# Kernel optimization log

Measured on AMD Instinct MI355X. Metric: run time of the kernel, lower is better.

The kernel has to match this reference:

```python
import jax, jax.numpy as jnp
import numpy as np
from jax import lax

DIM = 512
ATT_DIM = 512
N_HEADS = 8
HEAD_DIM = ATT_DIM // N_HEADS
SEQ = 4096


def q_rsqrt(x):
    # quake-style fast inverse sqrt with one Newton iteration (matches torch module)
    y = np.asarray((x,), dtype=np.float32)
    x2 = y * 0.5
    i = y.view(np.int32)
    i = np.right_shift(i, 1)
    i = 1597463007 - i
    y = i.view(np.float32)
    y = y * (1.5 - x2 * y * y)
    return float(y[0])

SCALING = q_rsqrt(HEAD_DIM)  # fast-approx 1/sqrt(head_dim)

# Schraudolph fast-exp constants (pulp-trainlib fastexp_gist)
GIST_A = 12102203.17133801  # 2^23 / ln(2)
GIST_B = 1064986823.0       # bias with correction term
GIST_C = 8388608.0          # underflow cutoff -> 0
GIST_D = 2139095040.0       # overflow clamp (float32 inf bits)


def fastexp_gist(x):
    t = GIST_A * x + GIST_B
    t = jnp.where(t < GIST_C, 0.0, jnp.where(t > GIST_D, GIST_D, t))
    return lax.bitcast_convert_type(t.astype(jnp.int32), jnp.float32)


def softmax_fastexp(s):
    m = jnp.max(s, axis=-1, keepdims=True)
    e = fastexp_gist(s - m)
    return e / jnp.sum(e, axis=-1, keepdims=True)


def setup_inputs() -> dict:
    key = jax.random.key(0)
    ks = jax.random.split(key, 8)
    std = 0.02
    return {
        "x": jax.random.normal(ks[0], (SEQ, DIM), dtype=jnp.float32),
        "Wq": jax.random.normal(ks[1], (ATT_DIM, DIM), dtype=jnp.float32) * std,
        "bq": jnp.zeros((ATT_DIM,), dtype=jnp.float32),
        "Wk": jax.random.normal(ks[2], (ATT_DIM, DIM), dtype=jnp.float32) * std,
        "bk": jnp.zeros((ATT_DIM,), dtype=jnp.float32),
        "Wv": jax.random.normal(ks[3], (ATT_DIM, DIM), dtype=jnp.float32) * std,
        "bv": jnp.zeros((ATT_DIM,), dtype=jnp.float32),
        "Wout": jax.random.normal(ks[4], (DIM, ATT_DIM), dtype=jnp.float32) * std,
        "tgt_len": SEQ,
    }


def reference(x, Wq, bq, Wk, bk, Wv, bv, Wout, tgt_len):
    # projections (torch Linear: y = x @ W.T + b)
    q = (x @ Wq.T + bq).reshape(tgt_len, N_HEADS, HEAD_DIM).transpose(1, 0, 2)  # [H,L,d]
    k = (x @ Wk.T + bk).reshape(tgt_len, N_HEADS, HEAD_DIM).transpose(1, 0, 2)
    v = (x @ Wv.T + bv).reshape(tgt_len, N_HEADS, HEAD_DIM).transpose(1, 0, 2)
    scores = jnp.einsum('hld,hmd->hlm', q, k) * SCALING  # [H,L,L]
    probs = softmax_fastexp(scores)
    out = jnp.einsum('hlm,hmd->hld', probs, v)           # [H,L,d]
    out = out.transpose(1, 0, 2).reshape(tgt_len, ATT_DIM)
    return out @ Wout.T  # proj_out has no bias
```

## Files before the change

kernel.cpp:

```cpp
#include <hip/hip_runtime.h>
#include <hip/hip_bf16.h>
#include <string.h>

#define SEQ 4096
#define DIM 512
#define NH  8
#define HD  64
#define SEQP (SEQ + 128)
#define NT  (SEQ/64)
#define KSPLIT 4
#define KCHUNK (SEQ/KSPLIT)
#define KTILES (KCHUNK/64)

typedef __attribute__((ext_vector_type(4))) float  f32x4;
typedef __attribute__((ext_vector_type(8))) short  bf16x8;
typedef __attribute__((ext_vector_type(4))) short  s16x4;
typedef __attribute__((ext_vector_type(2))) unsigned int u32x2;

__device__ __forceinline__ unsigned short f2bfh(float f){
    union { __hip_bfloat16 h; unsigned short u; } cv;
    cv.h = __float2bfloat16(f);
    return cv.u;
}

__device__ __forceinline__ bf16x8 cvt8(f32x4 lo, f32x4 hi){
    bf16x8 r;
    r[0]=(short)f2bfh(lo[0]); r[1]=(short)f2bfh(lo[1]);
    r[2]=(short)f2bfh(lo[2]); r[3]=(short)f2bfh(lo[3]);
    r[4]=(short)f2bfh(hi[0]); r[5]=(short)f2bfh(hi[1]);
    r[6]=(short)f2bfh(hi[2]); r[7]=(short)f2bfh(hi[3]);
    return r;
}

__device__ __forceinline__ bf16x8 load8f(const float* p){
    f32x4 lo = *(const f32x4*)p;
    f32x4 hi = *(const f32x4*)(p+4);
    return cvt8(lo, hi);
}

#define FENCE_LDS() asm volatile("s_waitcnt lgkmcnt(0)" ::: "memory")

__global__ __launch_bounds__(256) void cvt5_kernel(
    const float* __restrict__ x,  const float* __restrict__ wq,
    const float* __restrict__ wk, const float* __restrict__ wv,
    const float* __restrict__ wo,
    unsigned short* __restrict__ xb,  unsigned short* __restrict__ wqb,
    unsigned short* __restrict__ wkb, unsigned short* __restrict__ wvb,
    unsigned short* __restrict__ wob)
{
    int b = blockIdx.x;
    const float* src; unsigned short* dst; int base;
    if (b < 1024){ src = x; dst = xb; base = b; }
    else {
        int t  = (b - 1024) >> 7;
        base   = (b - 1024) & 127;
        src = (t==0) ? wq  : (t==1) ? wk  : (t==2) ? wv  : wo;
        dst = (t==0) ? wqb : (t==1) ? wkb : (t==2) ? wvb : wob;
    }
    size_t i = ((size_t)base*256 + threadIdx.x)*8;
    f32x4 lo = *(const f32x4*)(src + i);
    f32x4 hi = *(const f32x4*)(src + i + 4);
    *(bf16x8*)(dst + i) = cvt8(lo, hi);
}

__global__ __launch_bounds__(256, 4) void proj_qkv_b_kernel(
    const unsigned short* __restrict__ xb,
    const unsigned short* __restrict__ Wqb, const float* __restrict__ bq,
    const unsigned short* __restrict__ Wkb, const float* __restrict__ bk,
    const unsigned short* __restrict__ Wvb, const float* __restrict__ bv,
    unsigned short* __restrict__ Qb, unsigned short* __restrict__ Kh,
    unsigned short* __restrict__ Vtp)
{
    __shared__ __align__(16) unsigned short xs[128*64];
    __shared__ __align__(16) unsigned short wsh[64*64];

    const int z = blockIdx.z;
    const unsigned short* W = (z==0) ? Wqb : ((z==1) ? Wkb : Wvb);
    const float* bb = (z==0) ? bq : ((z==1) ? bk : bv);
    const int tid = threadIdx.x;
    const int wv  = tid >> 6;
    const int l   = tid & 63;
    const int g   = l >> 4;
    const int l15 = l & 15;
    const int l7  = l15 & 7;
    const int r0b = blockIdx.x * 128;
    const int c0  = blockIdx.y * 64;
    const int hy  = blockIdx.y;

    const int sc  = tid & 7;
    const int sr  = tid >> 3;
    const int scs = (sc ^ (sr & 7)) * 8;

    f32x4 acc[2][4];
    #pragma unroll
    for(int s=0;s<2;s++)
        #pragma unroll
        for(int d=0;d<4;d++) acc[s][d] = (f32x4){0.f,0.f,0.f,0.f};

    bf16x8 xf[4], wf[2];
    #pragma unroll
    for(int j=0;j<4;j++)
        xf[j] = *(const bf16x8*)(xb + (size_t)(r0b + sr + 32*j)*DIM + sc*8);
    #pragma unroll
    for(int j=0;j<2;j++)
        wf[j] = *(const bf16x8*)(W + (size_t)(c0 + sr + 32*j)*DIM + sc*8);

    for(int t=0;t<8;t++){
        #pragma unroll
        for(int j=0;j<4;j++)
            *(bf16x8*)&xs[(sr + 32*j)*64 + scs] = xf[j];
        #pragma unroll
        for(int j=0;j<2;j++)
            *(bf16x8*)&wsh[(sr + 32*j)*64 + scs] = wf[j];
        __syncthreads();
        if(t+1 < 8){
            const int kt = (t+1)*64;
            #pragma unroll
            for(int j=0;j<4;j++)
                xf[j] = *(const bf16x8*)(xb + (size_t)(r0b + sr + 32*j)*DIM + kt + sc*8);
            #pragma unroll
            for(int j=0;j<2;j++)
                wf[j] = *(const bf16x8*)(W + (size_t)(c0 + sr + 32*j)*DIM + kt + sc*8);
        }
        #pragma unroll
        for(int kh=0;kh<2;kh++){
            bf16x8 a[2];
            #pragma unroll
            for(int s=0;s<2;s++){
                const int row = wv*32 + s*16 + l15;
                a[s] = *(const bf16x8*)&xs[row*64 + (((kh*4+g) ^ l7)*8)];
            }
            #pragma unroll
            for(int d=0;d<4;d++){
                const int row = d*16 + l15;
                bf16x8 b = *(const bf16x8*)&wsh[row*64 + (((kh*4+g) ^ l7)*8)];
                #pragma unroll
                for(int s=0;s<2;s++)
                    acc[s][d] = __builtin_amdgcn_mfma_f32_16x16x32_bf16(a[s], b, acc[s][d], 0,0,0);
            }
        }
        __syncthreads();
    }

    const int r0 = r0b + wv*32;
    #pragma unroll
    for(int d=0;d<4;d++){
        float bias = bb[c0 + d*16 + l15];
        #pragma unroll
        for(int s=0;s<2;s++){
            if(z == 2){
                s16x4 pk;
                #pragma unroll
                for(int r=0;r<4;r++) pk[r] = (short)f2bfh(acc[s][d][r] + bias);
                *(s16x4*)(Vtp + ((size_t)hy*HD + d*16+l15)*SEQP + r0 + s*16 + g*4) = pk;
            } else if(z == 1){
                #pragma unroll
                for(int r=0;r<4;r++)
                    Kh[((size_t)hy*SEQ + r0+s*16+g*4+r)*HD + d*16 + l15] =
                        f2bfh(acc[s][d][r] + bias);
            } else {
                #pragma unroll
                for(int r=0;r<4;r++)
                    Qb[(size_t)(r0+s*16+g*4+r)*DIM + c0 + d*16 + l15] =
                        f2bfh(acc[s][d][r] + bias);
            }
        }
    }
}

__global__ __launch_bounds__(256) void proj_qkv_kernel(
    const float* __restrict__ x,
    const float* __restrict__ Wq, const float* __restrict__ bq,
    const float* __restrict__ Wk, const float* __restrict__ bk,
    const float* __restrict__ Wv, const float* __restrict__ bv,
    unsigned short* __restrict__ Qb, unsigned short* __restrict__ Kh,
    unsigned short* __restrict__ Vtp)
{
    const int z = blockIdx.z;
    const float* W  = (z==0) ? Wq : ((z==1) ? Wk : Wv);
    const float* bb = (z==0) ? bq : ((z==1) ? bk : bv);
    const int wv  = threadIdx.x >> 6;
    const int l   = threadIdx.x & 63;
    const int g   = l >> 4;
    const int l15 = l & 15;
    const int r0  = blockIdx.x * 128 + wv * 32;
    const int c0  = blockIdx.y * 64;
    const int hy  = blockIdx.y;

    f32x4 acc[2][4];
    #pragma unroll
    for(int s=0;s<2;s++)
        #pragma unroll
        for(int d=0;d<4;d++) acc[s][d] = (f32x4){0.f,0.f,0.f,0.f};

    for(int kt=0; kt<DIM; kt+=32){
        bf16x8 a[2];
        #pragma unroll
        for(int s=0;s<2;s++)
            a[s] = load8f(x + (size_t)(r0+s*16+l15)*DIM + kt + g*8);
        #pragma unroll
        for(int d=0;d<4;d++){
            bf16x8 b = load8f(W + (size_t)(c0+d*16+l15)*DIM + kt + g*8);
            #pragma unroll
            for(int s=0;s<2;s++)
                acc[s][d] = __builtin_amdgcn_mfma_f32_16x16x32_bf16(a[s], b, acc[s][d], 0,0,0);
        }
    }

    #pragma unroll
    for(int d=0;d<4;d++){
        float bias = bb[c0 + d*16 + l15];
        #pragma unroll
        for(int s=0;s<2;s++){
            if(z == 2){
                s16x4 pk;
                #pragma unroll
                for(int r=0;r<4;r++) pk[r] = (short)f2bfh(acc[s][d][r] + bias);
                *(s16x4*)(Vtp + ((size_t)hy*HD + d*16+l15)*SEQP + r0 + s*16 + g*4) = pk;
            } else if(z == 1){
                #pragma unroll
                for(int r=0;r<4;r++)
                    Kh[((size_t)hy*SEQ + r0+s*16+g*4+r)*HD + d*16 + l15] =
                        f2bfh(acc[s][d][r] + bias);
            } else {
                #pragma unroll
                for(int r=0;r<4;r++)
                    Qb[(size_t)(r0+s*16+g*4+r)*DIM + c0 + d*16 + l15] =
                        f2bfh(acc[s][d][r] + bias);
            }
        }
    }
}

__global__ __launch_bounds__(512, 4) void attn_max_kernel(
    const unsigned short* __restrict__ Qb,
    const unsigned short* __restrict__ Kh,
    float* __restrict__ Pm)
{
    __shared__ __align__(16) unsigned short kb[2][64*64];

    const int tid = threadIdx.x;
    const int wv  = tid >> 6;
    const int l   = tid & 63;
    const int g   = l >> 4;
    const int l15 = l & 15;
    const int l7  = l15 & 7;
    const int h   = blockIdx.x & 7;
    const int kz  = (blockIdx.x >> 3) & 3;
    const int Rw  = (blockIdx.x >> 5) * 256 + wv * 32;
    const int kbase = kz * KCHUNK;

    const unsigned short* Khh = Kh + (size_t)h*SEQ*HD;
    const int sr  = tid >> 3, sc = tid & 7;
    const int scs = (sc ^ (sr & 7)) * 8;
    const int lA  = sr*64 + scs;

    bf16x8 aq[2][2];
    #pragma unroll
    for(int s=0;s<2;s++)
        #pragma unroll
        for(int kh=0;kh<2;kh++)
            aq[s][kh] = *(const bf16x8*)(Qb + (size_t)(Rw+s*16+l15)*DIM + h*HD + kh*32 + g*8);

    float mx[2];
    mx[0] = mx[1] = -3.0e38f;

    bf16x8 krA = *(const bf16x8*)(Khh + (size_t)(kbase+sr)*HD + sc*8);
    *(bf16x8*)&kb[0][lA] = krA;
    __syncthreads();

    for(int t=0;t<KTILES;t++){
        const int cur = t & 1;
        if(t+1 < KTILES)
            krA = *(const bf16x8*)(Khh + (size_t)(kbase+(t+1)*64+sr)*HD + sc*8);
        #pragma unroll
        for(int ks=0;ks<4;ks++){
            const int krow = ks*16 + l15;
            bf16x8 b0 = *(const bf16x8*)&kb[cur][krow*64 + ((g     ^ l7)*8)];
            bf16x8 b1 = *(const bf16x8*)&kb[cur][krow*64 + (((4+g) ^ l7)*8)];
            __builtin_amdgcn_s_setprio(1);
            #pragma unroll
            for(int s=0;s<2;s++){
                f32x4 acc = (f32x4){0.f,0.f,0.f,0.f};
                acc = __builtin_amdgcn_mfma_f32_16x16x32_bf16(b0, aq[s][0], acc, 0,0,0);
                acc = __builtin_amdgcn_mfma_f32_16x16x32_bf16(b1, aq[s][1], acc, 0,0,0);
                #pragma unroll
                for(int r=0;r<4;r++) mx[s] = fmaxf(mx[s], acc[r]);
            }
            __builtin_amdgcn_s_setprio(0);
        }
        if(t+1 < KTILES)
            *(bf16x8*)&kb[cur^1][lA] = krA;
        __syncthreads();
    }
    #pragma unroll
    for(int s=0;s<2;s++){
        mx[s] = fmaxf(mx[s], __shfl_xor(mx[s], 16, 64));
        mx[s] = fmaxf(mx[s], __shfl_xor(mx[s], 32, 64));
    }

    if(l < 16){
        Pm[(size_t)(h*KSPLIT + kz)*SEQ + Rw + l15]      = mx[0];
        Pm[(size_t)(h*KSPLIT + kz)*SEQ + Rw + 16 + l15] = mx[1];
    }
}

#define PSTRIDE 68

__global__ __launch_bounds__(512, 4) void attn_pv_kernel(
    const unsigned short* __restrict__ Qb,
    const unsigned short* __restrict__ Kh,
    const unsigned short* __restrict__ Vtp,
    const float* __restrict__ Pm,
    float* __restrict__ numf,
    float* __restrict__ denf,
    float k1f)
{
    __shared__ __align__(16) unsigned short kb[2][64*64];
    __shared__ __align__(16) unsigned short vb[2][64*64];
    __shared__ __align__(16) unsigned short pb[8][32*PSTRIDE];

    const int tid = threadIdx.x;
    const int wv  = tid >> 6;
    const int l   = tid & 63;
    const int g   = l >> 4;
    const int l15 = l & 15;
    const int l7  = l15 & 7;
    const int h   = blockIdx.x & 7;
    const int kz  = (blockIdx.x >> 3) & 3;
    const int Rw  = (blockIdx.x >> 5) * 256 + wv * 32;
    const int kbase = kz * KCHUNK;

    const unsigned short* Khh = Kh  + (size_t)h*SEQ*HD;
    const unsigned short* Vh  = Vtp + (size_t)h*HD*SEQP;

    const int sr  = tid >> 3, sc = tid & 7;
    const int scs = (sc ^ (sr & 7)) * 8;
    const int lA  = sr*64 + scs;

    bf16x8 aq[2][2];
    #pragma unroll
    for(int s=0;s<2;s++)
        #pragma unroll
        for(int kh=0;kh<2;kh++)
            aq[s][kh] = *(const bf16x8*)(Qb + (size_t)(Rw+s*16+l15)*DIM + h*HD + kh*32 + g*8);

    float crow[2];
    #pragma unroll
    for(int s=0;s<2;s++){
        const int row = Rw + s*16 + l15;
        float m = Pm[(size_t)(h*KSPLIT+0)*SEQ + row];
        m = fmaxf(m, Pm[(size_t)(h*KSPLIT+1)*SEQ + row]);
        m = fmaxf(m, Pm[(size_t)(h*KSPLIT+2)*SEQ + row]);
        m = fmaxf(m, Pm[(size_t)(h*KSPLIT+3)*SEQ + row]);
        crow[s] = 1064986823.0f - k1f*m;
    }

    f32x4 oacc[2][4];
    #pragma unroll
    for(int s=0;s<2;s++)
        #pragma unroll
        for(int d=0;d<4;d++) oacc[s][d] = (f32x4){0.f,0.f,0.f,0.f};
    f32x4 dacc[2];
    dacc[0] = (f32x4){0.f,0.f,0.f,0.f};
    dacc[1] = (f32x4){0.f,0.f,0.f,0.f};

    bf16x8 ones;
    #pragma unroll
    for(int j=0;j<8;j++) ones[j] = (short)0x3F80;

    bf16x8 krA = *(const bf16x8*)(Khh + (size_t)(kbase+sr)*HD + sc*8);
    bf16x8 vrA = *(const bf16x8*)(Vh  + (size_t)sr*SEQP + kbase + sc*8);
    *(bf16x8*)&kb[0][lA] = krA;
    *(bf16x8*)&vb[0][lA] = vrA;
    __syncthreads();

    for(int t=0;t<KTILES;t++){
        const int cur = t & 1;
        if(t+1 < KTILES){
            const int k0n = kbase + (t+1)*64;
            krA = *(const bf16x8*)(Khh + (size_t)(k0n+sr)*HD + sc*8);
            vrA = *(const bf16x8*)(Vh  + (size_t)sr*SEQP + k0n + sc*8);
        }
        #pragma unroll
        for(int ks=0;ks<4;ks++){
            const int krow = ks*16 + l15;
            bf16x8 b0 = *(const bf16x8*)&kb[cur][krow*64 + ((g     ^ l7)*8)];
            bf16x8 b1 = *(const bf16x8*)&kb[cur][krow*64 + (((4+g) ^ l7)*8)];
            #pragma unroll
            for(int s=0;s<2;s++){
                f32x4 acc = (f32x4){0.f,0.f,0.f,0.f};
                __builtin_amdgcn_s_setprio(1);
                acc = __builtin_amdgcn_mfma_f32_16x16x32_bf16(b0, aq[s][0], acc, 0,0,0);
                acc = __builtin_amdgcn_mfma_f32_16x16x32_bf16(b1, aq[s][1], acc, 0,0,0);
                __builtin_amdgcn_s_setprio(0);
                unsigned int w0, w1;
                {
                    float t0 = fmaf(k1f, acc[0], crow[s]);
                    float t1 = fmaf(k1f, acc[1], crow[s]);
                    float t2 = fmaf(k1f, acc[2], crow[s]);
                    float t3 = fmaf(k1f, acc[3], crow[s]);
                    unsigned int p0 = f2bfh(__int_as_float((int)t0));
                    unsigned int p1 = f2bfh(__int_as_float((int)t1));
                    unsigned int p2 = f2bfh(__int_as_float((int)t2));
                    unsigned int p3 = f2bfh(__int_as_float((int)t3));
                    w0 = p0 | (p1 << 16);
                    w1 = p2 | (p3 << 16);
                }
                u32x2 pw; pw[0] = w0; pw[1] = w1;
                *(u32x2*)&pb[wv][(s*16+l15)*PSTRIDE + ks*16 + g*4] = pw;
            }
        }
        FENCE_LDS();

        __builtin_amdgcn_s_setprio(1);
        #pragma unroll
        for(int ks2=0; ks2<2; ks2++){
            bf16x8 pa[2];
            #pragma unroll
            for(int s=0;s<2;s++)
                pa[s] = *(const bf16x8*)&pb[wv][(s*16+l15)*PSTRIDE + ks2*32 + g*8];
            #pragma unroll
            for(int s=0;s<2;s++)
                dacc[s] = __builtin_amdgcn_mfma_f32_16x16x32_bf16(pa[s], ones, dacc[s], 0,0,0);
            #pragma unroll
            for(int d=0;d<4;d++){
                const int vrow = d*16 + l15;
                bf16x8 bv_ = *(const bf16x8*)&vb[cur][vrow*64 + (((ks2*4+g) ^ l7)*8)];
                #pragma unroll
                for(int s=0;s<2;s++)
                    oacc[s][d] = __builtin_amdgcn_mfma_f32_16x16x32_bf16(pa[s], bv_, oacc[s][d], 0,0,0);
            }
        }
        __builtin_amdgcn_s_setprio(0);

        if(t+1 < KTILES){
            *(bf16x8*)&kb[cur^1][lA] = krA;
            *(bf16x8*)&vb[cur^1][lA] = vrA;
        }
        __syncthreads();
    }

    #pragma unroll
    for(int s=0;s<2;s++)
        #pragma unroll
        for(int d=0;d<4;d++)
            #pragma unroll
            for(int r=0;r<4;r++)
                numf[(size_t)kz*SEQ*DIM + (size_t)(Rw+s*16+g*4+r)*DIM + h*HD + d*16 + l15]
                    = oacc[s][d][r];
    if(l15 == 0){
        #pragma unroll
        for(int s=0;s<2;s++)
            #pragma unroll
            for(int r=0;r<4;r++)
                denf[(size_t)kz*SEQ*NH + (size_t)(Rw+s*16+g*4+r)*NH + h] = dacc[s][r];
    }
}

__global__ __launch_bounds__(256) void attn_merge_kernel(
    const float* __restrict__ numf,
    const float* __restrict__ denf,
    unsigned short* __restrict__ Ab)
{
    const size_t NS = (size_t)SEQ*DIM;
    int idx = blockIdx.x*256 + threadIdx.x;
    int row = idx >> 7;
    int dg  = (idx & 127) << 2;
    int h   = dg >> 6;

    float d0 = denf[(size_t)0*SEQ*NH + (size_t)row*NH + h];
    float d1 = denf[(size_t)1*SEQ*NH + (size_t)row*NH + h];
    float d2 = denf[(size_t)2*SEQ*NH + (size_t)row*NH + h];
    float d3 = denf[(size_t)3*SEQ*NH + (size_t)row*NH + h];
    float inv = 1.0f / (((d0 + d1) + d2) + d3);

    f32x4 n0 = *(const f32x4*)(numf + 0*NS + (size_t)row*DIM + dg);
    f32x4 n1 = *(const f32x4*)(numf + 1*NS + (size_t)row*DIM + dg);
    f32x4 n2 = *(const f32x4*)(numf + 2*NS + (size_t)row*DIM + dg);
    f32x4 n3 = *(const f32x4*)(numf + 3*NS + (size_t)row*DIM + dg);
    f32x4 s = ((n0 + n1) + n2) + n3;

    s16x4 o;
    #pragma unroll
    for(int j=0;j<4;j++) o[j] = (short)f2bfh(s[j] * inv);
    *(s16x4*)(Ab + (size_t)row*DIM + dg) = o;
}

__global__ __launch_bounds__(256, 2) void attn_kernel(
    const unsigned short* __restrict__ Qb,
    const unsigned short* __restrict__ Kh,
    const unsigned short* __restrict__ Vtp,
    unsigned short* __restrict__ Ab,
    float k1f)
{
    __shared__ __align__(16) unsigned short kbf[2][64*64];
    __shared__ __align__(16) unsigned short vbf[2][64*64];
    __shared__ __align__(16) unsigned short pbf[4][16*68];

    const int tid = threadIdx.x;
    const int wv  = tid >> 6;
    const int l   = tid & 63;
    const int g   = l >> 4;
    const int l15 = l & 15;
    const int l7  = l15 & 7;
    const int h   = blockIdx.x & 7;
    const int Rw  = (blockIdx.x >> 3) * 64 + wv * 16;

    const unsigned short* Khh = Kh  + (size_t)h*SEQ*HD;
    const unsigned short* Vh  = Vtp + (size_t)h*HD*SEQP;

    const int sr  = tid >> 3;
    const int sc  = tid & 7;
    const int scs = (sc ^ (sr & 7)) * 8;
    const int ldsA = sr*64 + scs;
    const int ldsB = (sr+32)*64 + scs;

    bf16x8 aq[2];
    #pragma unroll
    for(int kh=0;kh<2;kh++)
        aq[kh] = *(const bf16x8*)(Qb + (size_t)(Rw+l15)*DIM + h*HD + kh*32 + g*8);

    bf16x8 krA, krB, vrA, vrB;

    float mx[4];
    mx[0]=mx[1]=mx[2]=mx[3]=-3.0e38f;

    krA = *(const bf16x8*)(Khh + (size_t)sr*HD      + sc*8);
    krB = *(const bf16x8*)(Khh + (size_t)(sr+32)*HD + sc*8);
    *(bf16x8*)&kbf[0][ldsA] = krA;
    *(bf16x8*)&kbf[0][ldsB] = krB;
    __syncthreads();

    for(int t=0;t<NT;t++){
        const int cur = t & 1;
        if(t+1 < NT){
            const unsigned short* kp = Khh + (size_t)((t+1)*64)*HD;
            krA = *(const bf16x8*)(kp + (size_t)sr*HD      + sc*8);
            krB = *(const bf16x8*)(kp + (size_t)(sr+32)*HD + sc*8);
        }
        #pragma unroll
        for(int ks=0;ks<4;ks++){
            const int krow = ks*16 + l15;
            bf16x8 b0 = *(const bf16x8*)&kbf[cur][krow*64 + ((g     ^ l7)*8)];
            bf16x8 b1 = *(const bf16x8*)&kbf[cur][krow*64 + (((4+g) ^ l7)*8)];
            f32x4 acc = (f32x4){0.f,0.f,0.f,0.f};
            acc = __builtin_amdgcn_mfma_f32_16x16x32_bf16(aq[0], b0, acc, 0,0,0);
            acc = __builtin_amdgcn_mfma_f32_16x16x32_bf16(aq[1], b1, acc, 0,0,0);
            #pragma unroll
            for(int r=0;r<4;r++) mx[r] = fmaxf(mx[r], acc[r]);
        }
        if(t+1 < NT){
            *(bf16x8*)&kbf[cur^1][ldsA] = krA;
            *(bf16x8*)&kbf[cur^1][ldsB] = krB;
        }
        __syncthreads();
    }
    #pragma unroll
    for(int off=1; off<16; off<<=1)
        #pragma unroll
        for(int r=0;r<4;r++)
            mx[r] = fmaxf(mx[r], __shfl_xor(mx[r], off, 64));
    float crow[4];
    #pragma unroll
    for(int r=0;r<4;r++) crow[r] = 1064986823.0f - k1f*mx[r];

    f32x4 oacc[4];
    #pragma unroll
    for(int d=0;d<4;d++) oacc[d] = (f32x4){0.f,0.f,0.f,0.f};
    f32x4 dacc = (f32x4){0.f,0.f,0.f,0.f};

    bf16x8 ones;
    #pragma unroll
    for(int j=0;j<8;j++) ones[j] = (short)0x3F80;

    krA = *(const bf16x8*)(Khh + (size_t)sr*HD        + sc*8);
    krB = *(const bf16x8*)(Khh + (size_t)(sr+32)*HD   + sc*8);
    vrA = *(const bf16x8*)(Vh  + (size_t)sr*SEQP      + sc*8);
    vrB = *(const bf16x8*)(Vh  + (size_t)(sr+32)*SEQP + sc*8);
    *(bf16x8*)&kbf[0][ldsA] = krA;  *(bf16x8*)&kbf[0][ldsB] = krB;
    *(bf16x8*)&vbf[0][ldsA] = vrA;  *(bf16x8*)&vbf[0][ldsB] = vrB;
    __syncthreads();

    for(int t=0;t<NT;t++){
        const int cur = t & 1;
        if(t+1 < NT){
            const int k0n = (t+1)*64;
            krA = *(const bf16x8*)(Khh + (size_t)(k0n + sr)*HD    + sc*8);
            krB = *(const bf16x8*)(Khh + (size_t)(k0n + sr+32)*HD + sc*8);
            vrA = *(const bf16x8*)(Vh  + (size_t)sr*SEQP      + k0n + sc*8);
            vrB = *(const bf16x8*)(Vh  + (size_t)(sr+32)*SEQP + k0n + sc*8);
        }
        #pragma unroll
        for(int ks=0;ks<4;ks++){
            const int krow = ks*16 + l15;
            bf16x8 b0 = *(const bf16x8*)&kbf[cur][krow*64 + ((g     ^ l7)*8)];
            bf16x8 b1 = *(const bf16x8*)&kbf[cur][krow*64 + (((4+g) ^ l7)*8)];
            f32x4 acc = (f32x4){0.f,0.f,0.f,0.f};
            acc = __builtin_amdgcn_mfma_f32_16x16x32_bf16(aq[0], b0, acc, 0,0,0);
            acc = __builtin_amdgcn_mfma_f32_16x16x32_bf16(aq[1], b1, acc, 0,0,0);
            #pragma unroll
            for(int r=0;r<4;r++){
                float tt = fmaf(k1f, acc[r], crow[r]);
                pbf[wv][(g*4+r)*68 + ks*16 + l15] = f2bfh(__int_as_float((int)tt));
            }
        }
        FENCE_LDS();

        #pragma unroll
        for(int ks2=0; ks2<2; ks2++){
            bf16x8 pa = *(const bf16x8*)&pbf[wv][l15*68 + ks2*32 + g*8];
            dacc = __builtin_amdgcn_mfma_f32_16x16x32_bf16(pa, ones, dacc, 0,0,0);
            #pragma unroll
            for(int d=0;d<4;d++){
                const int vrow = d*16 + l15;
                bf16x8 bv_ = *(const bf16x8*)&vbf[cur][vrow*64 + (((ks2*4+g) ^ l7)*8)];
                oacc[d] = __builtin_amdgcn_mfma_f32_16x16x32_bf16(pa, bv_, oacc[d], 0,0,0);
            }
        }
        if(t+1 < NT){
            *(bf16x8*)&kbf[cur^1][ldsA] = krA;  *(bf16x8*)&kbf[cur^1][ldsB] = krB;
            *(bf16x8*)&vbf[cur^1][ldsA] = vrA;  *(bf16x8*)&vbf[cur^1][ldsB] = vrB;
        }
        __syncthreads();
    }

    float inv[4];
    #pragma unroll
    for(int r=0;r<4;r++) inv[r] = 1.0f / dacc[r];
    #pragma unroll
    for(int d=0;d<4;d++)
        #pragma unroll
        for(int r=0;r<4;r++)
            Ab[(size_t)(Rw + g*4 + r)*DIM + h*HD + d*16 + l15] =
                f2bfh(oacc[d][r] * inv[r]);
}

__global__ __launch_bounds__(256) void proj_out_b_kernel(
    const unsigned short* __restrict__ Ab,
    const unsigned short* __restrict__ Wob,
    float* __restrict__ out)
{
    const int wv  = threadIdx.x >> 6;
    const int l   = threadIdx.x & 63;
    const int g   = l >> 4;
    const int l15 = l & 15;
    const int r0  = blockIdx.x * 128 + wv * 32;
    const int c0  = blockIdx.y * 64;

    f32x4 acc[2][4];
    #pragma unroll
    for(int s=0;s<2;s++)
        #pragma unroll
        for(int d=0;d<4;d++) acc[s][d] = (f32x4){0.f,0.f,0.f,0.f};

    for(int kt=0; kt<DIM; kt+=32){
        bf16x8 a[2];
        #pragma unroll
        for(int s=0;s<2;s++)
            a[s] = *(const bf16x8*)(Ab + (size_t)(r0+s*16+l15)*DIM + kt + g*8);
        #pragma unroll
        for(int d=0;d<4;d++){
            bf16x8 b = *(const bf16x8*)(Wob + (size_t)(c0+d*16+l15)*DIM + kt + g*8);
            #pragma unroll
            for(int s=0;s<2;s++)
                acc[s][d] = __builtin_amdgcn_mfma_f32_16x16x32_bf16(a[s], b, acc[s][d], 0,0,0);
        }
    }

    #pragma unroll
    for(int s=0;s<2;s++)
        #pragma unroll
        for(int d=0;d<4;d++)
            #pragma unroll
            for(int r=0;r<4;r++)
                out[(size_t)(r0+s*16+g*4+r)*DIM + c0 + d*16 + l15] = acc[s][d][r];
}

__global__ __launch_bounds__(256) void proj_out_kernel(
    const unsigned short* __restrict__ Ab,
    const float* __restrict__ Wout,
    float* __restrict__ out)
{
    const int wv  = threadIdx.x >> 6;
    const int l   = threadIdx.x & 63;
    const int g   = l >> 4;
    const int l15 = l & 15;
    const int r0  = blockIdx.x * 128 + wv * 32;
    const int c0  = blockIdx.y * 64;

    f32x4 acc[2][4];
    #pragma unroll
    for(int s=0;s<2;s++)
        #pragma unroll
        for(int d=0;d<4;d++) acc[s][d] = (f32x4){0.f,0.f,0.f,0.f};

    for(int kt=0; kt<DIM; kt+=32){
        bf16x8 a[2];
        #pragma unroll
        for(int s=0;s<2;s++)
            a[s] = *(const bf16x8*)(Ab + (size_t)(r0+s*16+l15)*DIM + kt + g*8);
        #pragma unroll
        for(int d=0;d<4;d++){
            bf16x8 b = load8f(Wout + (size_t)(c0+d*16+l15)*DIM + kt + g*8);
            #pragma unroll
            for(int s=0;s<2;s++)
                acc[s][d] = __builtin_amdgcn_mfma_f32_16x16x32_bf16(a[s], b, acc[s][d], 0,0,0);
        }
    }

    #pragma unroll
    for(int s=0;s<2;s++)
        #pragma unroll
        for(int d=0;d<4;d++)
            #pragma unroll
            for(int r=0;r<4;r++)
                out[(size_t)(r0+s*16+g*4+r)*DIM + c0 + d*16 + l15] = acc[s][d][r];
}

extern "C" void kernel_launch(void* const* d_in, const int* in_sizes, int n_in,
                              void* d_out, int out_size, void* d_ws, size_t ws_size,
                              hipStream_t stream)
{
    const float* x    = (const float*)d_in[0];
    const float* Wq   = (const float*)d_in[1];
    const float* bq   = (const float*)d_in[2];
    const float* Wk   = (const float*)d_in[3];
    const float* bk   = (const float*)d_in[4];
    const float* Wv   = (const float*)d_in[5];
    const float* bv   = (const float*)d_in[6];
    const float* Wout = (const float*)d_in[7];
    float* out = (float*)d_out;

    unsigned short* Qb  = (unsigned short*)d_ws;
    unsigned short* Kh  = Qb  + (size_t)SEQ*DIM;
    unsigned short* Vtp = Kh  + (size_t)NH*SEQ*HD;
    unsigned short* Ab  = Vtp + (size_t)NH*HD*SEQP;
    unsigned short* xb  = Ab  + (size_t)SEQ*DIM;
    unsigned short* Wqb = xb  + (size_t)SEQ*DIM;
    unsigned short* Wkb = Wqb + (size_t)DIM*DIM;
    unsigned short* Wvb = Wkb + (size_t)DIM*DIM;
    unsigned short* Wob = Wvb + (size_t)DIM*DIM;
    float* Pm   = (float*)(Wob + (size_t)DIM*DIM);
    float* numf = Pm   + (size_t)NH*KSPLIT*SEQ;
    float* denf = numf + (size_t)KSPLIT*SEQ*DIM;

    const size_t needed_bf16 = ((size_t)SEQ*DIM*4 + (size_t)NH*HD*SEQP
                                + (size_t)DIM*DIM*4) * 2;
    const size_t needed_f32  = ((size_t)NH*KSPLIT*SEQ + (size_t)KSPLIT*SEQ*DIM
                                + (size_t)KSPLIT*SEQ*NH) * 4;
    const size_t needed_split = needed_bf16 + needed_f32;

    float xx = 64.0f;
    float x2 = xx * 0.5f;
    int ii; memcpy(&ii, &xx, 4);
    ii = 1597463007 - (ii >> 1);
    float y; memcpy(&y, &ii, 4);
    y = y * (1.5f - x2 * y * y);
    const float scaling = y;
    const float k1f = 12102203.17133801f * scaling;

    if(ws_size >= needed_split){
        cvt5_kernel<<<dim3(1536), 256, 0, stream>>>(
            x, Wq, Wk, Wv, Wout, xb, Wqb, Wkb, Wvb, Wob);
        proj_qkv_b_kernel<<<dim3(SEQ/128, DIM/64, 3), 256, 0, stream>>>(
            xb, Wqb, bq, Wkb, bk, Wvb, bv, Qb, Kh, Vtp);
        attn_max_kernel<<<dim3((SEQ/256)*NH*KSPLIT), 512, 0, stream>>>(Qb, Kh, Pm);
        attn_pv_kernel<<<dim3((SEQ/256)*NH*KSPLIT), 512, 0, stream>>>(
            Qb, Kh, Vtp, Pm, numf, denf, k1f);
        attn_merge_kernel<<<dim3(SEQ*DIM/4/256), 256, 0, stream>>>(numf, denf, Ab);
        proj_out_b_kernel<<<dim3(SEQ/128, DIM/64), 256, 0, stream>>>(Ab, Wob, out);
    } else if(ws_size >= needed_bf16){
        cvt5_kernel<<<dim3(1536), 256, 0, stream>>>(
            x, Wq, Wk, Wv, Wout, xb, Wqb, Wkb, Wvb, Wob);
        proj_qkv_b_kernel<<<dim3(SEQ/128, DIM/64, 3), 256, 0, stream>>>(
            xb, Wqb, bq, Wkb, bk, Wvb, bv, Qb, Kh, Vtp);
        attn_kernel<<<dim3((SEQ/64)*NH), 256, 0, stream>>>(Qb, Kh, Vtp, Ab, k1f);
        proj_out_b_kernel<<<dim3(SEQ/128, DIM/64), 256, 0, stream>>>(Ab, Wob, out);
    } else {
        proj_qkv_kernel<<<dim3(SEQ/128, DIM/64, 3), 256, 0, stream>>>(
            x, Wq, bq, Wk, bk, Wv, bv, Qb, Kh, Vtp);
        attn_kernel<<<dim3((SEQ/64)*NH), 256, 0, stream>>>(Qb, Kh, Vtp, Ab, k1f);
        proj_out_kernel<<<dim3(SEQ/128, DIM/64), 256, 0, stream>>>(Ab, Wout, out);
    }
}
```

Baseline: 105.1 us.

## Split max pass into more key chunks, drop setprio, stage proj_out via LDS

The row-max kernel now splits the keys into 8 chunks instead of 4, doubling the number of blocks to 1024 for better occupancy. The pv kernel reduces over all 8 partial maxima. The s_setprio hints are removed from both attention kernels. The output projection now stages 128x64 activation tiles and 64x64 weight tiles in swizzled LDS with register prefetch, replacing per-lane direct global loads, and its launch bounds are raised. Together these should cut memory traffic in the projection and add parallelism to the max pass, at the cost of more partial-max traffic and LDS syncs.

```diff
diff --git a/kernel.cpp b/kernel.cpp
--- a/kernel.cpp
+++ b/kernel.cpp
@@ -11,6 +11,9 @@
 #define KSPLIT 4
 #define KCHUNK (SEQ/KSPLIT)
 #define KTILES (KCHUNK/64)
+#define PMSPLIT 8
+#define KCHUNK_A (SEQ/PMSPLIT)
+#define KTILES_A (KCHUNK_A/64)
 
 typedef __attribute__((ext_vector_type(4))) float  f32x4;
 typedef __attribute__((ext_vector_type(8))) short  bf16x8;
@@ -246,9 +249,9 @@
     const int l15 = l & 15;
     const int l7  = l15 & 7;
     const int h   = blockIdx.x & 7;
-    const int kz  = (blockIdx.x >> 3) & 3;
-    const int Rw  = (blockIdx.x >> 5) * 256 + wv * 32;
-    const int kbase = kz * KCHUNK;
+    const int kz  = (blockIdx.x >> 3) & 7;
+    const int Rw  = (blockIdx.x >> 6) * 256 + wv * 32;
+    const int kbase = kz * KCHUNK_A;
 
     const unsigned short* Khh = Kh + (size_t)h*SEQ*HD;
     const int sr  = tid >> 3, sc = tid & 7;
@@ -269,16 +272,15 @@
     *(bf16x8*)&kb[0][lA] = krA;
     __syncthreads();
 
-    for(int t=0;t<KTILES;t++){
+    for(int t=0;t<KTILES_A;t++){
         const int cur = t & 1;
-        if(t+1 < KTILES)
+        if(t+1 < KTILES_A)
             krA = *(const bf16x8*)(Khh + (size_t)(kbase+(t+1)*64+sr)*HD + sc*8);
         #pragma unroll
         for(int ks=0;ks<4;ks++){
             const int krow = ks*16 + l15;
             bf16x8 b0 = *(const bf16x8*)&kb[cur][krow*64 + ((g     ^ l7)*8)];
             bf16x8 b1 = *(const bf16x8*)&kb[cur][krow*64 + (((4+g) ^ l7)*8)];
-            __builtin_amdgcn_s_setprio(1);
             #pragma unroll
             for(int s=0;s<2;s++){
                 f32x4 acc = (f32x4){0.f,0.f,0.f,0.f};
@@ -287,9 +289,8 @@
                 #pragma unroll
                 for(int r=0;r<4;r++) mx[s] = fmaxf(mx[s], acc[r]);
             }
-            __builtin_amdgcn_s_setprio(0);
-        }
-        if(t+1 < KTILES)
+        }
+        if(t+1 < KTILES_A)
             *(bf16x8*)&kb[cur^1][lA] = krA;
         __syncthreads();
     }
@@ -300,8 +301,8 @@
     }
 
     if(l < 16){
-        Pm[(size_t)(h*KSPLIT + kz)*SEQ + Rw + l15]      = mx[0];
-        Pm[(size_t)(h*KSPLIT + kz)*SEQ + Rw + 16 + l15] = mx[1];
+        Pm[(size_t)(h*PMSPLIT + kz)*SEQ + Rw + l15]      = mx[0];
+        Pm[(size_t)(h*PMSPLIT + kz)*SEQ + Rw + 16 + l15] = mx[1];
     }
 }
 
@@ -349,10 +350,10 @@
     #pragma unroll
     for(int s=0;s<2;s++){
         const int row = Rw + s*16 + l15;
-        float m = Pm[(size_t)(h*KSPLIT+0)*SEQ + row];
-        m = fmaxf(m, Pm[(size_t)(h*KSPLIT+1)*SEQ + row]);
-        m = fmaxf(m, Pm[(size_t)(h*KSPLIT+2)*SEQ + row]);
-        m = fmaxf(m, Pm[(size_t)(h*KSPLIT+3)*SEQ + row]);
+        float m = Pm[(size_t)(h*PMSPLIT+0)*SEQ + row];
+        #pragma unroll
+        for(int p=1;p<PMSPLIT;p++)
+            m = fmaxf(m, Pm[(size_t)(h*PMSPLIT+p)*SEQ + row]);
         crow[s] = 1064986823.0f - k1f*m;
     }
 
@@ -390,10 +391,8 @@
             #pragma unroll
             for(int s=0;s<2;s++){
                 f32x4 acc = (f32x4){0.f,0.f,0.f,0.f};
-                __builtin_amdgcn_s_setprio(1);
                 acc = __builtin_amdgcn_mfma_f32_16x16x32_bf16(b0, aq[s][0], acc, 0,0,0);
                 acc = __builtin_amdgcn_mfma_f32_16x16x32_bf16(b1, aq[s][1], acc, 0,0,0);
-                __builtin_amdgcn_s_setprio(0);
                 unsigned int w0, w1;
                 {
                     float t0 = fmaf(k1f, acc[0], crow[s]);
@@ -636,38 +635,79 @@
                 f2bfh(oacc[d][r] * inv[r]);
 }
 
-__global__ __launch_bounds__(256) void proj_out_b_kernel(
+__global__ __launch_bounds__(256, 4) void proj_out_b_kernel(
     const unsigned short* __restrict__ Ab,
     const unsigned short* __restrict__ Wob,
     float* __restrict__ out)
 {
-    const int wv  = threadIdx.x >> 6;
-    const int l   = threadIdx.x & 63;
+    __shared__ __align__(16) unsigned short xs[128*64];
+    __shared__ __align__(16) unsigned short wsh[64*64];
+
+    const int tid = threadIdx.x;
+    const int wv  = tid >> 6;
+    const int l   = tid & 63;
     const int g   = l >> 4;
     const int l15 = l & 15;
-    const int r0  = blockIdx.x * 128 + wv * 32;
+    const int l7  = l15 & 7;
+    const int r0b = blockIdx.x * 128;
     const int c0  = blockIdx.y * 64;
 
+    const int sc  = tid & 7;
+    const int sr  = tid >> 3;
+    const int scs = (sc ^ (sr & 7)) * 8;
+
     f32x4 acc[2][4];
     #pragma unroll
     for(int s=0;s<2;s++)
         #pragma unroll
         for(int d=0;d<4;d++) acc[s][d] = (f32x4){0.f,0.f,0.f,0.f};
 
-    for(int kt=0; kt<DIM; kt+=32){
-        bf16x8 a[2];
-        #pragma unroll
-        for(int s=0;s<2;s++)
-            a[s] = *(const bf16x8*)(Ab + (size_t)(r0+s*16+l15)*DIM + kt + g*8);
-        #pragma unroll
-        for(int d=0;d<4;d++){
-            bf16x8 b = *(const bf16x8*)(Wob + (size_t)(c0+d*16+l15)*DIM + kt + g*8);
-            #pragma unroll
-            for(int s=0;s<2;s++)
-                acc[s][d] = __builtin_amdgcn_mfma_f32_16x16x32_bf16(a[s], b, acc[s][d], 0,0,0);
-        }
-    }
-
+    bf16x8 xf[4], wf[2];
+    #pragma unroll
+    for(int j=0;j<4;j++)
+        xf[j] = *(const bf16x8*)(Ab + (size_t)(r0b + sr + 32*j)*DIM + sc*8);
+    #pragma unroll
+    for(int j=0;j<2;j++)
+        wf[j] = *(const bf16x8*)(Wob + (size_t)(c0 + sr + 32*j)*DIM + sc*8);
+
+    for(int t=0;t<8;t++){
+        #pragma unroll
+        for(int j=0;j<4;j++)
+            *(bf16x8*)&xs[(sr + 32*j)*64 + scs] = xf[j];
+        #pragma unroll
+        for(int j=0;j<2;j++)
+            *(bf16x8*)&wsh[(sr + 32*j)*64 + scs] = wf[j];
+        __syncthreads();
+        if(t+1 < 8){
+            const int kt = (t+1)*64;
+            #pragma unroll
+            for(int j=0;j<4;j++)
+                xf[j] = *(const bf16x8*)(Ab + (size_t)(r0b + sr + 32*j)*DIM + kt + sc*8);
+            #pragma unroll
+            for(int j=0;j<2;j++)
+                wf[j] = *(const bf16x8*)(Wob + (size_t)(c0 + sr + 32*j)*DIM + kt + sc*8);
+        }
+        #pragma unroll
+        for(int kh=0;kh<2;kh++){
+            bf16x8 a[2];
+            #pragma unroll
+            for(int s=0;s<2;s++){
+                const int row = wv*32 + s*16 + l15;
+                a[s] = *(const bf16x8*)&xs[row*64 + (((kh*4+g) ^ l7)*8)];
+            }
+            #pragma unroll
+            for(int d=0;d<4;d++){
+                const int row = d*16 + l15;
+                bf16x8 b = *(const bf16x8*)&wsh[row*64 + (((kh*4+g) ^ l7)*8)];
+                #pragma unroll
+                for(int s=0;s<2;s++)
+                    acc[s][d] = __builtin_amdgcn_mfma_f32_16x16x32_bf16(a[s], b, acc[s][d], 0,0,0);
+            }
+        }
+        __syncthreads();
+    }
+
+    const int r0 = r0b + wv*32;
     #pragma unroll
     for(int s=0;s<2;s++)
         #pragma unroll
@@ -742,12 +782,12 @@
     unsigned short* Wvb = Wkb + (size_t)DIM*DIM;
     unsigned short* Wob = Wvb + (size_t)DIM*DIM;
     float* Pm   = (float*)(Wob + (size_t)DIM*DIM);
-    float* numf = Pm   + (size_t)NH*KSPLIT*SEQ;
+    float* numf = Pm   + (size_t)NH*PMSPLIT*SEQ;
     float* denf = numf + (size_t)KSPLIT*SEQ*DIM;
 
     const size_t needed_bf16 = ((size_t)SEQ*DIM*4 + (size_t)NH*HD*SEQP
                                 + (size_t)DIM*DIM*4) * 2;
-    const size_t needed_f32  = ((size_t)NH*KSPLIT*SEQ + (size_t)KSPLIT*SEQ*DIM
+    const size_t needed_f32  = ((size_t)NH*PMSPLIT*SEQ + (size_t)KSPLIT*SEQ*DIM
                                 + (size_t)KSPLIT*SEQ*NH) * 4;
     const size_t needed_split = needed_bf16 + needed_f32;
 
@@ -765,7 +805,7 @@
             x, Wq, Wk, Wv, Wout, xb, Wqb, Wkb, Wvb, Wob);
         proj_qkv_b_kernel<<<dim3(SEQ/128, DIM/64, 3), 256, 0, stream>>>(
             xb, Wqb, bq, Wkb, bk, Wvb, bv, Qb, Kh, Vtp);
-        attn_max_kernel<<<dim3((SEQ/256)*NH*KSPLIT), 512, 0, stream>>>(Qb, Kh, Pm);
+        attn_max_kernel<<<dim3((SEQ/256)*NH*PMSPLIT), 512, 0, stream>>>(Qb, Kh, Pm);
         attn_pv_kernel<<<dim3((SEQ/256)*NH*KSPLIT), 512, 0, stream>>>(
             Qb, Kh, Vtp, Pm, numf, denf, k1f);
         attn_merge_kernel<<<dim3(SEQ*DIM/4/256), 256, 0, stream>>>(numf, denf, Ab);
```

Result: faster. 100.6 us (-4.3%).
